# Performance work log

Measured on AMD Instinct MI355X. Metric: run time of the kernel, lower is better.

The kernel has to match this reference:

```python
import jax, jax.numpy as jnp
import numpy as np

K = 32  # neighbors per query point


def _gather_points(x, idx):
    # x: [B, N, D], idx: [B, M, k] -> [B, M, k, D]
    B, M, k = idx.shape
    D = x.shape[-1]
    flat = jnp.take_along_axis(x, idx.reshape(B, M * k, 1), axis=1)
    return flat.reshape(B, M, k, D)


def setup_inputs() -> dict:
    key = jax.random.key(0)
    k1, k2, k3, k4, k5 = jax.random.split(key, 5)
    B, N, M, Cin = 16, 4096, 1024, 64
    pos = jax.random.normal(k1, (B, N, 3), dtype=jnp.float32)
    features = jax.random.normal(k2, (B, N, Cin), dtype=jnp.float32)
    idx = jax.random.randint(k3, (B, M), 0, N, dtype=jnp.int64)
    # 1x1 conv2d MLP params: (Cin+3) -> 64 -> 128 (use_xyz adds 3 channels)
    W1 = jax.random.normal(k4, (Cin + 3, 64), dtype=jnp.float32) * (1.0 / np.sqrt(Cin + 3))
    b1 = jnp.zeros((64,), dtype=jnp.float32)
    W2 = jax.random.normal(k5, (64, 128), dtype=jnp.float32) * (1.0 / np.sqrt(64))
    b2 = jnp.zeros((128,), dtype=jnp.float32)
    return {"pos": pos, "features": features, "W1": W1, "b1": b1,
            "W2": W2, "b2": b2, "idx": idx}


def reference(pos, features, W1, b1, W2, b2, idx):
    # pos: [B,N,3], features: [B,N,C], idx: [B,M] query-point indices
    pos_q = jnp.take_along_axis(pos, idx[..., None], axis=1)  # [B,M,3]
    # squared-distance knn: [B,M,N]
    d2 = (jnp.sum(pos_q ** 2, -1, keepdims=True)
          + jnp.sum(pos ** 2, -1)[:, None, :]
          - 2.0 * jnp.einsum("bmd,bnd->bmn", pos_q, pos))
    _, nn_idx = jax.lax.top_k(-d2, K)  # [B,M,K] nearest neighbors
    grouped_pos = _gather_points(pos, nn_idx)          # [B,M,K,3]
    grouped_feat = _gather_points(features, nn_idx)    # [B,M,K,C]
    rel = grouped_pos - pos_q[:, :, None, :]           # recenter groups
    x = jnp.concatenate([rel, grouped_feat], axis=-1)  # [B,M,K,C+3] (use_xyz)
    # 1x1 conv2d MLP == per-point linear + ReLU on channel dim
    h = jax.nn.relu(jnp.einsum("bmkc,cd->bmkd", x, W1) + b1)
    h = jax.nn.relu(jnp.einsum("bmkc,cd->bmkd", h, W2) + b2)
    out = jnp.max(h, axis=-2)  # max over K neighbors -> [B,M,128]
    return (pos_q, out)
```

## Files before the change

kernel.cpp:

```cpp
#include <hip/hip_runtime.h>

#define NPTS  4096
#define MQ    1024
#define BATCH 16
#define KNN   32
#define CIN   64
#define H1D   64
#define H2D   128

typedef _Float16 half8 __attribute__((ext_vector_type(8)));
typedef float    floatx4 __attribute__((ext_vector_type(4)));

#define WS_NN_BYTES ((size_t)BATCH * MQ * KNN * 4)
#define W1F_HALVES  (3 * 4 * 64 * 8)
#define W2F_HALVES  (2 * 8 * 64 * 8)
#define WS_P4_OFF   (WS_NN_BYTES + (W1F_HALVES + W2F_HALVES) * 2)

__global__ __launch_bounds__(256) void wprep_kernel(
    const float* __restrict__ W1, const float* __restrict__ W2,
    const float* __restrict__ pos,
    _Float16* __restrict__ wout, float4* __restrict__ pos4)
{
    const int gid = blockIdx.x * 256 + threadIdx.x;
    if (gid < 768) {
        const int s = gid;
        const int kc = s >> 8, nt = (s >> 6) & 3, lane = s & 63;
        const int col = lane & 15, quad = lane >> 4;
        half8 ph;
#pragma unroll
        for (int j = 0; j < 8; ++j) {
            const int k = kc * 32 + quad * 8 + j;
            ph[j] = (k < 67) ? (_Float16)W1[k * H1D + nt * 16 + col] : (_Float16)0.0f;
        }
        *(half8*)(wout + (size_t)s * 8) = ph;
    } else if (gid < 1792) {
        const int s2 = gid - 768;
        const int kc2 = s2 >> 9, nt2 = (s2 >> 6) & 7, lane = s2 & 63;
        const int col = lane & 15, quad = lane >> 4;
        half8 ph;
#pragma unroll
        for (int j = 0; j < 8; ++j) {
            const int k = kc2 * 32 + quad * 8 + j;
            ph[j] = (_Float16)W2[k * H2D + nt2 * 16 + col];
        }
        *(half8*)(wout + (size_t)W1F_HALVES + (size_t)s2 * 8) = ph;
    } else {
        const int p = gid - 1792;
        if (p < BATCH * NPTS) {
            const float px = pos[p * 3 + 0], py = pos[p * 3 + 1], pz = pos[p * 3 + 2];
            float4 v;
            v.x = px; v.y = py; v.z = pz;
            v.w = __fadd_rn(__fadd_rn(__fmul_rn(px, px), __fmul_rn(py, py)),
                            __fmul_rn(pz, pz));
            pos4[p] = v;
        }
    }
}

__global__ __launch_bounds__(256, 4) void knn_kernel(
    const float4* __restrict__ pos4, const int* __restrict__ idx,
    float* __restrict__ pos_q, int* __restrict__ nn)
{
    const int KCAP = 512;
    const int bid = blockIdx.x;
    const int b   = bid >> 10;
    const int m   = bid & (MQ - 1);
    const int t   = threadIdx.x;
    const int wv  = t >> 6, lane = t & 63;

    __shared__ unsigned int gmin[64];
    __shared__ uint2 cand[512];
    __shared__ unsigned int sc[2];
    __shared__ unsigned long long w64[4];

    const float4* pb4 = pos4 + (size_t)b * NPTS;
    const int qn = idx[(size_t)b * MQ + m];
    const float4 qv = pb4[qn];
    const float qq = qv.w;

    if (t == 0) sc[1] = 0u;

    float4 p[16];
#pragma unroll
    for (int i = 0; i < 16; ++i) p[i] = pb4[i * 256 + t];

    unsigned int k[16];
    unsigned int lmin = 0xFFFFFFFFu;
#pragma unroll
    for (int i = 0; i < 16; ++i) {
        const float qp = __fadd_rn(__fadd_rn(__fmul_rn(qv.x, p[i].x), __fmul_rn(qv.y, p[i].y)),
                                   __fmul_rn(qv.z, p[i].z));
        const float d2 = __fsub_rn(__fadd_rn(qq, p[i].w), __fmul_rn(2.0f, qp));
        unsigned int u = __float_as_uint(d2);
        u = (u & 0x80000000u) ? ~u : (u | 0x80000000u);
        k[i] = u;
        lmin = min(lmin, u);
    }

    lmin = min(lmin, (unsigned int)__shfl_xor((int)lmin, 1));
    lmin = min(lmin, (unsigned int)__shfl_xor((int)lmin, 2));
    if ((lane & 3) == 0) gmin[t >> 2] = lmin;
    __syncthreads();

    if (wv == 0) {
        const unsigned int g = gmin[lane];
        int rk = 0;
        for (int j = 0; j < 64; ++j) {
            const unsigned int gj = (unsigned int)__shfl((int)g, j);
            if (gj < g || (gj == g && j < lane)) ++rk;
        }
        if (rk == 31) sc[0] = g;
    }
    __syncthreads();
    const unsigned int T = sc[0];

#pragma unroll
    for (int i = 0; i < 16; ++i) {
        if (k[i] <= T) {
            const unsigned int slot = atomicAdd(&sc[1], 1u);
            if (slot < (unsigned)KCAP)
                cand[slot] = make_uint2(k[i], (unsigned int)(i * 256 + t));
        }
    }
    __syncthreads();
    const int candcnt = (int)sc[1];

    if (candcnt <= KCAP) {
        if (t < candcnt) {
            const uint2 my = cand[t];
            int rk = 0;
            for (int j = 0; j < candcnt; ++j) {
                const uint2 c = cand[j];
                if (c.x < my.x || (c.x == my.x && c.y < my.y)) ++rk;
            }
            if (rk < KNN) nn[(size_t)bid * KNN + rk] = (int)my.y;
        }
    } else {
        unsigned long long last = 0ull;
        for (int r = 0; r < KNN; ++r) {
            __syncthreads();
            unsigned long long best = ~0ull;
#pragma unroll
            for (int i = 0; i < 16; ++i) {
                const unsigned long long pk =
                    ((unsigned long long)k[i] << 32) | (unsigned int)(i * 256 + t);
                if ((r == 0 || pk > last) && pk < best) best = pk;
            }
#pragma unroll
            for (int off = 1; off < 64; off <<= 1) {
                const unsigned long long o = __shfl_xor(best, off);
                if (o < best) best = o;
            }
            if (lane == 0) w64[wv] = best;
            __syncthreads();
            if (t == 0) {
                unsigned long long bb = w64[0];
                for (int wi = 1; wi < 4; ++wi) if (w64[wi] < bb) bb = w64[wi];
                w64[0] = bb;
                nn[(size_t)bid * KNN + r] = (int)(bb & 0xFFFFFFFFu);
            }
            __syncthreads();
            last = w64[0];
        }
    }

    if (t == 0) {
        pos_q[(size_t)bid * 3 + 0] = qv.x;
        pos_q[(size_t)bid * 3 + 1] = qv.y;
        pos_q[(size_t)bid * 3 + 2] = qv.z;
    }
}

__global__ __launch_bounds__(256, 4) void mlp_kernel(
    const float4* __restrict__ pos4, const float* __restrict__ feat,
    const float* __restrict__ b1, const float* __restrict__ b2,
    const float* __restrict__ pos_q, const int* __restrict__ nn,
    const _Float16* __restrict__ wf, float* __restrict__ out)
{
    __shared__ _Float16 sh[4 * 3072];
    const int t = threadIdx.x;
    const int w = t >> 6, lane = t & 63;
    const int col = lane & 15, quad = lane >> 4;
    const int q = blockIdx.x * 4 + w;
    const int b = q >> 10;
    const int wbase = w * 3072;

    {
        const int r = t >> 1, h = t & 1;
        const int kk = r & 31;
        const int n = nn[(size_t)q * KNN + kk];
        const float4 pv = pos4[(size_t)b * NPTS + n];
        const float4* f4 = (const float4*)(feat + ((size_t)b * NPTS + n) * CIN);
        const int mt = kk >> 4, lrow = kk & 15;
        if (h == 0) {
            float4 ff[12];
#pragma unroll
            for (int ii = 0; ii < 12; ++ii) ff[ii] = f4[ii];
            float rel[3];
            rel[0] = pv.x - pos_q[(size_t)q * 3 + 0];
            rel[1] = pv.y - pos_q[(size_t)q * 3 + 1];
            rel[2] = pv.z - pos_q[(size_t)q * 3 + 2];
#pragma unroll
            for (int ci = 0; ci < 6; ++ci) {
                half8 ph;
#pragma unroll
                for (int jj = 0; jj < 8; ++jj) {
                    const int c = ci * 8 + jj;
                    float v;
                    if (c < 3) v = rel[c];
                    else {
                        const int fc = c - 3;
                        const float4 vv = ff[fc >> 2];
                        v = ((fc & 3) == 0) ? vv.x : ((fc & 3) == 1) ? vv.y
                          : ((fc & 3) == 2) ? vv.z : vv.w;
                    }
                    ph[jj] = (_Float16)v;
                }
                const int kc = ci >> 2, qd = ci & 3;
                *(half8*)&sh[wbase + ((kc * 2 + mt) * 64 + qd * 16 + lrow) * 8] = ph;
            }
        } else {
            float4 ff[5];
#pragma unroll
            for (int ii = 0; ii < 5; ++ii) ff[ii] = f4[11 + ii];
#pragma unroll
            for (int ci = 6; ci < 12; ++ci) {
                half8 ph;
#pragma unroll
                for (int jj = 0; jj < 8; ++jj) {
                    const int c = ci * 8 + jj;
                    float v = 0.0f;
                    if (c < 67) {
                        const int fc = c - 3;
                        const float4 vv = ff[(fc >> 2) - 11];
                        v = ((fc & 3) == 0) ? vv.x : ((fc & 3) == 1) ? vv.y
                          : ((fc & 3) == 2) ? vv.z : vv.w;
                    }
                    ph[jj] = (_Float16)v;
                }
                const int kc = ci >> 2, qd = ci & 3;
                *(half8*)&sh[wbase + ((kc * 2 + mt) * 64 + qd * 16 + lrow) * 8] = ph;
            }
        }
    }

    half8 af[3][2];
#pragma unroll
    for (int kc = 0; kc < 3; ++kc)
#pragma unroll
        for (int mt = 0; mt < 2; ++mt)
            af[kc][mt] = *(const half8*)&sh[wbase + ((kc * 2 + mt) * 64 + lane) * 8];

    half8 w1f[3][4];
#pragma unroll
    for (int kc = 0; kc < 3; ++kc)
#pragma unroll
        for (int nt = 0; nt < 4; ++nt)
            w1f[kc][nt] = *(const half8*)(wf + (size_t)((kc * 4 + nt) * 64 + lane) * 8);

#pragma unroll
    for (int nt = 0; nt < 4; ++nt) {
        const float bv = b1[nt * 16 + col];
        floatx4 acc0 = {bv, bv, bv, bv}, acc1 = acc0;
#pragma unroll
        for (int kc = 0; kc < 3; ++kc) {
            acc0 = __builtin_amdgcn_mfma_f32_16x16x32_f16(af[kc][0], w1f[kc][nt], acc0, 0, 0, 0);
            acc1 = __builtin_amdgcn_mfma_f32_16x16x32_f16(af[kc][1], w1f[kc][nt], acc1, 0, 0, 0);
        }
        const int kc2 = nt >> 1;
        const int quad2 = (((nt & 1) * 16) + col) >> 3;
        const int j2 = col & 7;
#pragma unroll
        for (int mt = 0; mt < 2; ++mt) {
            const floatx4 a = mt ? acc1 : acc0;
#pragma unroll
            for (int reg = 0; reg < 4; ++reg) {
                const int row = quad * 4 + reg;
                sh[wbase + ((kc2 * 2 + mt) * 64 + quad2 * 16 + row) * 8 + j2] =
                    (_Float16)fmaxf(a[reg], 0.0f);
            }
        }
    }

    half8 a2[2][2];
#pragma unroll
    for (int kc2 = 0; kc2 < 2; ++kc2)
#pragma unroll
        for (int mt = 0; mt < 2; ++mt)
            a2[kc2][mt] = *(const half8*)&sh[wbase + ((kc2 * 2 + mt) * 64 + lane) * 8];

    half8 w2f[2][8];
#pragma unroll
    for (int kc2 = 0; kc2 < 2; ++kc2)
#pragma unroll
        for (int nt2 = 0; nt2 < 8; ++nt2)
            w2f[kc2][nt2] = *(const half8*)(wf + (size_t)W1F_HALVES
                                            + (size_t)((kc2 * 8 + nt2) * 64 + lane) * 8);

    float* oq = out + (size_t)q * H2D;
#pragma unroll
    for (int nt2 = 0; nt2 < 8; ++nt2) {
        const float bv = b2[nt2 * 16 + col];
        floatx4 acc0 = {bv, bv, bv, bv}, acc1 = acc0;
#pragma unroll
        for (int kc2 = 0; kc2 < 2; ++kc2) {
            acc0 = __builtin_amdgcn_mfma_f32_16x16x32_f16(a2[kc2][0], w2f[kc2][nt2], acc0, 0, 0, 0);
            acc1 = __builtin_amdgcn_mfma_f32_16x16x32_f16(a2[kc2][1], w2f[kc2][nt2], acc1, 0, 0, 0);
        }
        float mm = fmaxf(fmaxf(fmaxf(acc0[0], acc0[1]), fmaxf(acc0[2], acc0[3])),
                         fmaxf(fmaxf(acc1[0], acc1[1]), fmaxf(acc1[2], acc1[3])));
        mm = fmaxf(mm, 0.0f);
        mm = fmaxf(mm, __shfl_xor(mm, 16));
        mm = fmaxf(mm, __shfl_xor(mm, 32));
        if (lane < 16) oq[nt2 * 16 + lane] = mm;
    }
}

extern "C" void kernel_launch(void* const* d_in, const int* in_sizes, int n_in,
                              void* d_out, int out_size, void* d_ws, size_t ws_size,
                              hipStream_t stream)
{
    const float* pos  = (const float*)d_in[0];
    const float* feat = (const float*)d_in[1];
    const float* W1   = (const float*)d_in[2];
    const float* b1   = (const float*)d_in[3];
    const float* W2   = (const float*)d_in[4];
    const float* b2   = (const float*)d_in[5];
    const int*   idx  = (const int*)d_in[6];

    float* pos_q = (float*)d_out;
    float* out   = (float*)d_out + (size_t)BATCH * MQ * 3;
    int*      nn = (int*)d_ws;
    _Float16* wf = (_Float16*)((char*)d_ws + WS_NN_BYTES);
    float4*   p4 = (float4*)((char*)d_ws + WS_P4_OFF);

    const int prep_threads = 1792 + BATCH * NPTS;
    wprep_kernel<<<(prep_threads + 255) / 256, 256, 0, stream>>>(W1, W2, pos, wf, p4);
    knn_kernel<<<BATCH * MQ, 256, 0, stream>>>(p4, idx, pos_q, nn);
    mlp_kernel<<<BATCH * MQ / 4, 256, 0, stream>>>(p4, feat, b1, b2,
                                                   pos_q, nn, wf, out);
}
```

Before: 208.1 us.

## Stage batch points in LDS and process one query per wavefront in kNN

The kNN kernel now uses 512 blocks. Each block stages the 4096 points of one batch in shared memory once, and each wavefront handles 8 queries in turn. The threshold is found with a wave-level bitonic sort of per-lane minima, and candidates are compacted with a prefix scan instead of LDS atomics and block barriers. This removes redundant global loads of the point cloud for every query and cuts block-wide synchronisation. In exchange it uses 64KB of LDS and 64 key registers per thread, which lowers occupancy, and the grid is much smaller, which may underfill the GPU.

```diff
diff --git a/kernel.cpp b/kernel.cpp
--- a/kernel.cpp
+++ b/kernel.cpp
@@ -57,117 +57,110 @@
     }
 }
 
-__global__ __launch_bounds__(256, 4) void knn_kernel(
+__global__ __launch_bounds__(256) void knn_kernel(
     const float4* __restrict__ pos4, const int* __restrict__ idx,
     float* __restrict__ pos_q, int* __restrict__ nn)
 {
-    const int KCAP = 512;
+    const int CCAP = 128;
     const int bid = blockIdx.x;
-    const int b   = bid >> 10;
-    const int m   = bid & (MQ - 1);
+    const int b   = bid >> 5;
     const int t   = threadIdx.x;
-    const int wv  = t >> 6, lane = t & 63;
-
-    __shared__ unsigned int gmin[64];
-    __shared__ uint2 cand[512];
-    __shared__ unsigned int sc[2];
-    __shared__ unsigned long long w64[4];
+    const int w   = t >> 6, lane = t & 63;
+
+    __shared__ float4 slab[NPTS];
+    __shared__ uint2  cand[4][128];
 
     const float4* pb4 = pos4 + (size_t)b * NPTS;
-    const int qn = idx[(size_t)b * MQ + m];
-    const float4 qv = pb4[qn];
-    const float qq = qv.w;
-
-    if (t == 0) sc[1] = 0u;
-
-    float4 p[16];
-#pragma unroll
-    for (int i = 0; i < 16; ++i) p[i] = pb4[i * 256 + t];
-
-    unsigned int k[16];
-    unsigned int lmin = 0xFFFFFFFFu;
-#pragma unroll
-    for (int i = 0; i < 16; ++i) {
-        const float qp = __fadd_rn(__fadd_rn(__fmul_rn(qv.x, p[i].x), __fmul_rn(qv.y, p[i].y)),
-                                   __fmul_rn(qv.z, p[i].z));
-        const float d2 = __fsub_rn(__fadd_rn(qq, p[i].w), __fmul_rn(2.0f, qp));
-        unsigned int u = __float_as_uint(d2);
-        u = (u & 0x80000000u) ? ~u : (u | 0x80000000u);
-        k[i] = u;
-        lmin = min(lmin, u);
-    }
-
-    lmin = min(lmin, (unsigned int)__shfl_xor((int)lmin, 1));
-    lmin = min(lmin, (unsigned int)__shfl_xor((int)lmin, 2));
-    if ((lane & 3) == 0) gmin[t >> 2] = lmin;
+#pragma unroll
+    for (int r = 0; r < 16; ++r) slab[r * 256 + t] = pb4[r * 256 + t];
     __syncthreads();
 
-    if (wv == 0) {
-        const unsigned int g = gmin[lane];
-        int rk = 0;
-        for (int j = 0; j < 64; ++j) {
-            const unsigned int gj = (unsigned int)__shfl((int)g, j);
-            if (gj < g || (gj == g && j < lane)) ++rk;
-        }
-        if (rk == 31) sc[0] = g;
-    }
-    __syncthreads();
-    const unsigned int T = sc[0];
-
-#pragma unroll
-    for (int i = 0; i < 16; ++i) {
-        if (k[i] <= T) {
-            const unsigned int slot = atomicAdd(&sc[1], 1u);
-            if (slot < (unsigned)KCAP)
-                cand[slot] = make_uint2(k[i], (unsigned int)(i * 256 + t));
-        }
-    }
-    __syncthreads();
-    const int candcnt = (int)sc[1];
-
-    if (candcnt <= KCAP) {
-        if (t < candcnt) {
-            const uint2 my = cand[t];
-            int rk = 0;
-            for (int j = 0; j < candcnt; ++j) {
-                const uint2 c = cand[j];
-                if (c.x < my.x || (c.x == my.x && c.y < my.y)) ++rk;
-            }
-            if (rk < KNN) nn[(size_t)bid * KNN + rk] = (int)my.y;
-        }
-    } else {
-        unsigned long long last = 0ull;
-        for (int r = 0; r < KNN; ++r) {
-            __syncthreads();
-            unsigned long long best = ~0ull;
-#pragma unroll
-            for (int i = 0; i < 16; ++i) {
-                const unsigned long long pk =
-                    ((unsigned long long)k[i] << 32) | (unsigned int)(i * 256 + t);
-                if ((r == 0 || pk > last) && pk < best) best = pk;
-            }
-#pragma unroll
-            for (int off = 1; off < 64; off <<= 1) {
-                const unsigned long long o = __shfl_xor(best, off);
-                if (o < best) best = o;
-            }
-            if (lane == 0) w64[wv] = best;
-            __syncthreads();
-            if (t == 0) {
-                unsigned long long bb = w64[0];
-                for (int wi = 1; wi < 4; ++wi) if (w64[wi] < bb) bb = w64[wi];
-                w64[0] = bb;
-                nn[(size_t)bid * KNN + r] = (int)(bb & 0xFFFFFFFFu);
-            }
-            __syncthreads();
-            last = w64[0];
-        }
-    }
-
-    if (t == 0) {
-        pos_q[(size_t)bid * 3 + 0] = qv.x;
-        pos_q[(size_t)bid * 3 + 1] = qv.y;
-        pos_q[(size_t)bid * 3 + 2] = qv.z;
+    for (int qi = 0; qi < 8; ++qi) {
+        const int m = (bid & 31) * 32 + w * 8 + qi;
+        const int q = b * MQ + m;
+        const int qn = idx[q];
+        const float4 qv = slab[qn];
+        const float qq = qv.w;
+
+        unsigned int k[64];
+        unsigned int lmin = 0xFFFFFFFFu;
+#pragma unroll
+        for (int i = 0; i < 64; ++i) {
+            const float4 p = slab[i * 64 + lane];
+            const float qp = __fadd_rn(__fadd_rn(__fmul_rn(qv.x, p.x), __fmul_rn(qv.y, p.y)),
+                                       __fmul_rn(qv.z, p.z));
+            const float d2 = __fsub_rn(__fadd_rn(qq, p.w), __fmul_rn(2.0f, qp));
+            unsigned int u = __float_as_uint(d2);
+            u = (u & 0x80000000u) ? ~u : (u | 0x80000000u);
+            k[i] = u;
+            lmin = min(lmin, u);
+        }
+
+        unsigned int v = lmin;
+#pragma unroll
+        for (int kk = 2; kk <= 64; kk <<= 1) {
+#pragma unroll
+            for (int j = kk >> 1; j > 0; j >>= 1) {
+                const unsigned int o = (unsigned int)__shfl_xor((int)v, j);
+                const bool keepSmall = (((lane & kk) == 0) == ((lane & j) == 0));
+                v = keepSmall ? min(v, o) : max(v, o);
+            }
+        }
+        const unsigned int T = (unsigned int)__shfl((int)v, 31);
+
+        int c = 0;
+#pragma unroll
+        for (int i = 0; i < 64; ++i) c += (k[i] <= T) ? 1 : 0;
+        int pre = c;
+#pragma unroll
+        for (int off = 1; off < 64; off <<= 1) {
+            const int o = __shfl_up(pre, off);
+            if (lane >= off) pre += o;
+        }
+        const int total = __shfl(pre, 63);
+
+        if (total <= CCAP) {
+            uint2* wc = cand[w];
+            int o = pre - c;
+#pragma unroll
+            for (int i = 0; i < 64; ++i) {
+                if (k[i] <= T) { wc[o] = make_uint2(k[i], (unsigned)(i * 64 + lane)); ++o; }
+            }
+            uint2 e0 = (lane < total) ? wc[lane] : make_uint2(0xFFFFFFFFu, 0xFFFFFFFFu);
+            uint2 e1 = (lane + 64 < total) ? wc[lane + 64] : make_uint2(0xFFFFFFFFu, 0xFFFFFFFFu);
+            int r0 = 0, r1 = 0;
+            for (int j = 0; j < total; ++j) {
+                const uint2 cj = wc[j];
+                r0 += (cj.x < e0.x || (cj.x == e0.x && cj.y < e0.y)) ? 1 : 0;
+                r1 += (cj.x < e1.x || (cj.x == e1.x && cj.y < e1.y)) ? 1 : 0;
+            }
+            if (lane < total && r0 < KNN)      nn[(size_t)q * KNN + r0] = (int)e0.y;
+            if (lane + 64 < total && r1 < KNN) nn[(size_t)q * KNN + r1] = (int)e1.y;
+        } else {
+            unsigned long long last = 0ull;
+            for (int r = 0; r < KNN; ++r) {
+                unsigned long long best = ~0ull;
+#pragma unroll
+                for (int i = 0; i < 64; ++i) {
+                    const unsigned long long pk =
+                        ((unsigned long long)k[i] << 32) | (unsigned)(i * 64 + lane);
+                    if ((r == 0 || pk > last) && pk < best) best = pk;
+                }
+#pragma unroll
+                for (int off = 1; off < 64; off <<= 1) {
+                    const unsigned long long ob = __shfl_xor(best, off);
+                    if (ob < best) best = ob;
+                }
+                if (lane == 0) nn[(size_t)q * KNN + r] = (int)(best & 0xFFFFFFFFu);
+                last = best;
+            }
+        }
+
+        if (lane == 0) {
+            pos_q[(size_t)q * 3 + 0] = qv.x;
+            pos_q[(size_t)q * 3 + 1] = qv.y;
+            pos_q[(size_t)q * 3 + 2] = qv.z;
+        }
     }
 }
 
@@ -336,7 +329,7 @@
 
     const int prep_threads = 1792 + BATCH * NPTS;
     wprep_kernel<<<(prep_threads + 255) / 256, 256, 0, stream>>>(W1, W2, pos, wf, p4);
-    knn_kernel<<<BATCH * MQ, 256, 0, stream>>>(p4, idx, pos_q, nn);
+    knn_kernel<<<512, 256, 0, stream>>>(p4, idx, pos_q, nn);
     mlp_kernel<<<BATCH * MQ / 4, 256, 0, stream>>>(p4, feat, b1, b2,
                                                    pos_q, nn, wf, out);
 }
```

After: 242.3 us. +16.4%, slower.

## Process four queries per KNN block reusing register-resident point cloud

Applied to the files above, without the earlier changes.

Each KNN block now handles four query points, loading the 4096 batch points into registers once and reusing them for every query, which cuts repeated global loads and block launch count by four. The serial 64-way rank threshold search is replaced by a wavefront bitonic sort. The candidate buffer is shrunk to 128 entries, so the slow iterative fallback runs whenever more candidates pass the threshold. Launch bounds for both kernels drop to 3 blocks per CU, trading occupancy for register headroom.

```diff
diff --git a/kernel.cpp b/kernel.cpp
--- a/kernel.cpp
+++ b/kernel.cpp
@@ -57,121 +57,130 @@
     }
 }
 
-__global__ __launch_bounds__(256, 4) void knn_kernel(
+#define QPB  4
+#define CCAP 128
+__global__ __launch_bounds__(256, 3) void knn_kernel(
     const float4* __restrict__ pos4, const int* __restrict__ idx,
     float* __restrict__ pos_q, int* __restrict__ nn)
 {
-    const int KCAP = 512;
     const int bid = blockIdx.x;
-    const int b   = bid >> 10;
-    const int m   = bid & (MQ - 1);
+    const int b   = bid >> 8;
+    const int mb  = (bid & 255) * QPB;
     const int t   = threadIdx.x;
     const int wv  = t >> 6, lane = t & 63;
 
     __shared__ unsigned int gmin[64];
-    __shared__ uint2 cand[512];
+    __shared__ uint2 cand[CCAP];
     __shared__ unsigned int sc[2];
     __shared__ unsigned long long w64[4];
 
     const float4* pb4 = pos4 + (size_t)b * NPTS;
-    const int qn = idx[(size_t)b * MQ + m];
-    const float4 qv = pb4[qn];
-    const float qq = qv.w;
-
-    if (t == 0) sc[1] = 0u;
 
     float4 p[16];
 #pragma unroll
     for (int i = 0; i < 16; ++i) p[i] = pb4[i * 256 + t];
 
-    unsigned int k[16];
-    unsigned int lmin = 0xFFFFFFFFu;
-#pragma unroll
-    for (int i = 0; i < 16; ++i) {
-        const float qp = __fadd_rn(__fadd_rn(__fmul_rn(qv.x, p[i].x), __fmul_rn(qv.y, p[i].y)),
-                                   __fmul_rn(qv.z, p[i].z));
-        const float d2 = __fsub_rn(__fadd_rn(qq, p[i].w), __fmul_rn(2.0f, qp));
-        unsigned int u = __float_as_uint(d2);
-        u = (u & 0x80000000u) ? ~u : (u | 0x80000000u);
-        k[i] = u;
-        lmin = min(lmin, u);
-    }
-
-    lmin = min(lmin, (unsigned int)__shfl_xor((int)lmin, 1));
-    lmin = min(lmin, (unsigned int)__shfl_xor((int)lmin, 2));
-    if ((lane & 3) == 0) gmin[t >> 2] = lmin;
-    __syncthreads();
-
-    if (wv == 0) {
-        const unsigned int g = gmin[lane];
-        int rk = 0;
-        for (int j = 0; j < 64; ++j) {
-            const unsigned int gj = (unsigned int)__shfl((int)g, j);
-            if (gj < g || (gj == g && j < lane)) ++rk;
-        }
-        if (rk == 31) sc[0] = g;
-    }
-    __syncthreads();
-    const unsigned int T = sc[0];
-
-#pragma unroll
-    for (int i = 0; i < 16; ++i) {
-        if (k[i] <= T) {
-            const unsigned int slot = atomicAdd(&sc[1], 1u);
-            if (slot < (unsigned)KCAP)
-                cand[slot] = make_uint2(k[i], (unsigned int)(i * 256 + t));
-        }
-    }
-    __syncthreads();
-    const int candcnt = (int)sc[1];
-
-    if (candcnt <= KCAP) {
-        if (t < candcnt) {
-            const uint2 my = cand[t];
-            int rk = 0;
-            for (int j = 0; j < candcnt; ++j) {
-                const uint2 c = cand[j];
-                if (c.x < my.x || (c.x == my.x && c.y < my.y)) ++rk;
-            }
-            if (rk < KNN) nn[(size_t)bid * KNN + rk] = (int)my.y;
-        }
-    } else {
-        unsigned long long last = 0ull;
-        for (int r = 0; r < KNN; ++r) {
-            __syncthreads();
-            unsigned long long best = ~0ull;
-#pragma unroll
-            for (int i = 0; i < 16; ++i) {
-                const unsigned long long pk =
-                    ((unsigned long long)k[i] << 32) | (unsigned int)(i * 256 + t);
-                if ((r == 0 || pk > last) && pk < best) best = pk;
-            }
-#pragma unroll
-            for (int off = 1; off < 64; off <<= 1) {
-                const unsigned long long o = __shfl_xor(best, off);
-                if (o < best) best = o;
-            }
-            if (lane == 0) w64[wv] = best;
-            __syncthreads();
-            if (t == 0) {
-                unsigned long long bb = w64[0];
-                for (int wi = 1; wi < 4; ++wi) if (w64[wi] < bb) bb = w64[wi];
-                w64[0] = bb;
-                nn[(size_t)bid * KNN + r] = (int)(bb & 0xFFFFFFFFu);
-            }
-            __syncthreads();
-            last = w64[0];
-        }
-    }
-
-    if (t == 0) {
-        pos_q[(size_t)bid * 3 + 0] = qv.x;
-        pos_q[(size_t)bid * 3 + 1] = qv.y;
-        pos_q[(size_t)bid * 3 + 2] = qv.z;
+    for (int qi = 0; qi < QPB; ++qi) {
+        const int q  = b * MQ + mb + qi;
+        const int qn = idx[q];
+        const float4 qv = pb4[qn];
+        const float qq = qv.w;
+
+        unsigned int k[16];
+        unsigned int lmin = 0xFFFFFFFFu;
+#pragma unroll
+        for (int i = 0; i < 16; ++i) {
+            const float qp = __fadd_rn(__fadd_rn(__fmul_rn(qv.x, p[i].x), __fmul_rn(qv.y, p[i].y)),
+                                       __fmul_rn(qv.z, p[i].z));
+            const float d2 = __fsub_rn(__fadd_rn(qq, p[i].w), __fmul_rn(2.0f, qp));
+            unsigned int u = __float_as_uint(d2);
+            u = (u & 0x80000000u) ? ~u : (u | 0x80000000u);
+            k[i] = u;
+            lmin = min(lmin, u);
+        }
+
+        lmin = min(lmin, (unsigned int)__shfl_xor((int)lmin, 1));
+        lmin = min(lmin, (unsigned int)__shfl_xor((int)lmin, 2));
+        if ((t & 3) == 0) gmin[t >> 2] = lmin;
+        if (t == 0) sc[1] = 0u;
+        __syncthreads();
+
+        if (wv == 0) {
+            unsigned int v = gmin[lane];
+#pragma unroll
+            for (int kk = 2; kk <= 64; kk <<= 1) {
+#pragma unroll
+                for (int j = kk >> 1; j > 0; j >>= 1) {
+                    const unsigned int o = (unsigned int)__shfl_xor((int)v, j);
+                    const bool keepSmall = (((lane & kk) == 0) == ((lane & j) == 0));
+                    v = keepSmall ? min(v, o) : max(v, o);
+                }
+            }
+            if (lane == 31) sc[0] = v;
+        }
+        __syncthreads();
+        const unsigned int T = sc[0];
+
+#pragma unroll
+        for (int i = 0; i < 16; ++i) {
+            if (k[i] <= T) {
+                const unsigned int slot = atomicAdd(&sc[1], 1u);
+                if (slot < (unsigned)CCAP)
+                    cand[slot] = make_uint2(k[i], (unsigned int)(i * 256 + t));
+            }
+        }
+        __syncthreads();
+        const int C = (int)sc[1];
+
+        if (C <= CCAP) {
+            if (t < C) {
+                const uint2 my = cand[t];
+                int rk = 0;
+                for (int j = 0; j < C; ++j) {
+                    const uint2 cj = cand[j];
+                    rk += (cj.x < my.x || (cj.x == my.x && cj.y < my.y)) ? 1 : 0;
+                }
+                if (rk < KNN) nn[(size_t)q * KNN + rk] = (int)my.y;
+            }
+        } else {
+            unsigned long long last = 0ull;
+            for (int r = 0; r < KNN; ++r) {
+                __syncthreads();
+                unsigned long long best = ~0ull;
+#pragma unroll
+                for (int i = 0; i < 16; ++i) {
+                    const unsigned long long pk =
+                        ((unsigned long long)k[i] << 32) | (unsigned int)(i * 256 + t);
+                    if ((r == 0 || pk > last) && pk < best) best = pk;
+                }
+#pragma unroll
+                for (int off = 1; off < 64; off <<= 1) {
+                    const unsigned long long ob = __shfl_xor(best, off);
+                    if (ob < best) best = ob;
+                }
+                if (lane == 0) w64[wv] = best;
+                __syncthreads();
+                if (t == 0) {
+                    unsigned long long bb = w64[0];
+                    for (int wi = 1; wi < 4; ++wi) if (w64[wi] < bb) bb = w64[wi];
+                    w64[0] = bb;
+                    nn[(size_t)q * KNN + r] = (int)(bb & 0xFFFFFFFFu);
+                }
+                __syncthreads();
+                last = w64[0];
+            }
+        }
+
+        if (t == 0) {
+            pos_q[(size_t)q * 3 + 0] = qv.x;
+            pos_q[(size_t)q * 3 + 1] = qv.y;
+            pos_q[(size_t)q * 3 + 2] = qv.z;
+        }
+        __syncthreads();
     }
 }
 
-__global__ __launch_bounds__(256, 4) void mlp_kernel(
+__global__ __launch_bounds__(256, 3) void mlp_kernel(
     const float4* __restrict__ pos4, const float* __restrict__ feat,
     const float* __restrict__ b1, const float* __restrict__ b2,
     const float* __restrict__ pos_q, const int* __restrict__ nn,
@@ -336,7 +345,7 @@
 
     const int prep_threads = 1792 + BATCH * NPTS;
     wprep_kernel<<<(prep_threads + 255) / 256, 256, 0, stream>>>(W1, W2, pos, wf, p4);
-    knn_kernel<<<BATCH * MQ, 256, 0, stream>>>(p4, idx, pos_q, nn);
+    knn_kernel<<<BATCH * MQ / QPB, 256, 0, stream>>>(p4, idx, pos_q, nn);
     mlp_kernel<<<BATCH * MQ / 4, 256, 0, stream>>>(p4, feat, b1, b2,
                                                    pos_q, nn, wf, out);
 }
```

Result: slower. 297.7 us (+43.1%).
